# Kernel optimization log

Measured on AMD Instinct MI355X. Metric: run time of the kernel, lower is better.

## Reference

```python
import jax, jax.numpy as jnp
import numpy as np

B, S, D = 4, 2048, 384
H, KVH, HD = 6, 2, 64
GROUPS = H // KVH  # 3
ROPE_THETA = 100000.0


def _rope_tables(seq_len, head_dim, theta):
    inv = 1.0 / (theta ** (np.arange(0, head_dim, 2, dtype=np.float32) / head_dim))
    t = np.arange(seq_len, dtype=np.float32)
    freqs = np.outer(t, inv)  # [S, HD//2]
    return jnp.asarray(np.cos(freqs)), jnp.asarray(np.sin(freqs))


def setup_inputs() -> dict:
    key = jax.random.key(0)
    ks = jax.random.split(key, 5)
    hidden_states = jax.random.normal(ks[0], (B, S, D), dtype=jnp.float32)
    Wq = jax.random.normal(ks[1], (D, H * HD), dtype=jnp.float32) * 0.02
    Wk = jax.random.normal(ks[2], (D, KVH * HD), dtype=jnp.float32) * 0.02
    Wv = jax.random.normal(ks[3], (D, KVH * HD), dtype=jnp.float32) * 0.02
    Wo = jax.random.normal(ks[4], (H * HD, D), dtype=jnp.float32) * 0.02
    freqs_cos, freqs_sin = _rope_tables(S, HD, ROPE_THETA)
    return {"hidden_states": hidden_states, "Wq": Wq, "Wk": Wk, "Wv": Wv,
            "Wo": Wo, "freqs_cos": freqs_cos, "freqs_sin": freqs_sin}


def _apply_rope(x, cos, sin):
    # x: [B, S, h, HD]; treat pairs (even, odd) as complex, multiply by e^{i theta}
    xr = x.reshape(*x.shape[:-1], HD // 2, 2)
    x0, x1 = xr[..., 0], xr[..., 1]
    c = cos[None, :, None, :]  # [1, S, 1, HD//2]
    s = sin[None, :, None, :]
    o0 = x0 * c - x1 * s
    o1 = x0 * s + x1 * c
    return jnp.stack([o0, o1], axis=-1).reshape(x.shape)


def reference(hidden_states, Wq, Wk, Wv, Wo, freqs_cos, freqs_sin):
    Bc, Sc, _ = hidden_states.shape
    q = (hidden_states @ Wq).reshape(Bc, Sc, H, HD)
    k = (hidden_states @ Wk).reshape(Bc, Sc, KVH, HD)
    v = (hidden_states @ Wv).reshape(Bc, Sc, KVH, HD)
    q = _apply_rope(q, freqs_cos, freqs_sin)
    k = _apply_rope(k, freqs_cos, freqs_sin)
    # repeat_interleave over the head dim (GQA group broadcast)
    k = jnp.repeat(k, GROUPS, axis=2)  # [B, S, H, HD]
    v = jnp.repeat(v, GROUPS, axis=2)
    scale = 1.0 / jnp.sqrt(jnp.float32(HD))
    scores = jnp.einsum('bqhd,bkhd->bhqk', q, k) * scale  # [B, H, S, S]
    attn = jax.nn.softmax(scores, axis=-1)
    out = jnp.einsum('bhqk,bkhd->bqhd', attn, v)  # [B, S, H, HD]
    out = out.reshape(Bc, Sc, H * HD)
    return out @ Wo
```

## Files before the change

kernel.cpp:

```cpp
#include <hip/hip_runtime.h>
#include <stdint.h>

#define BATCH   4
#define SEQ     2048
#define DMODEL  384
#define NHEAD   6
#define NKVH    2
#define HD      64
#define MTOK    (BATCH*SEQ)
#define NQKV    640
#define QSCALE  (0.125f * 1.4426950408889634f)

typedef __bf16 bf16x8 __attribute__((ext_vector_type(8)));
typedef float  f32x16 __attribute__((ext_vector_type(16)));

__device__ inline unsigned short f2bf(float f) {
  union { float f; unsigned int u; } v; v.f = f;
  return (unsigned short)((v.u + 0x7fffu + ((v.u >> 16) & 1u)) >> 16);
}
__device__ inline float bf2f(unsigned short b) {
  union { unsigned int u; float f; } v; v.u = ((unsigned int)b) << 16;
  return v.f;
}
__device__ inline unsigned int pack2bf(float a, float b) {
  return (unsigned int)f2bf(a) | ((unsigned int)f2bf(b) << 16);
}
__device__ inline unsigned int cvtpk(float lo, float hi) {
  unsigned int r;
  asm("v_cvt_pk_bf16_f32 %0, %1, %2" : "=v"(r) : "v"(lo), "v"(hi));
  return r;
}
__device__ inline float exp2_fast(float x) {
  float r;
  asm("v_exp_f32 %0, %1" : "=v"(r) : "v"(x));
  return r;
}

#define GLOAD16(gsrc, ldst) __builtin_amdgcn_global_load_lds( \
    (const __attribute__((address_space(1))) void*)(gsrc), \
    (__attribute__((address_space(3))) void*)(ldst), 16, 0, 0)

#define WAITV8() asm volatile("s_waitcnt vmcnt(8)" ::: "memory")
#define WAITV0() asm volatile("s_waitcnt vmcnt(0)" ::: "memory")

__global__ void prep_kernel(const float* __restrict__ X,
                            const float* __restrict__ Wq, const float* __restrict__ Wk,
                            const float* __restrict__ Wv, const float* __restrict__ Wo,
                            unsigned short* __restrict__ Xb,
                            unsigned short* __restrict__ WT,
                            unsigned short* __restrict__ WoT) {
  int idx = blockIdx.x * 256 + threadIdx.x;
  if (idx < (MTOK*DMODEL)/4) {
    float4 v = ((const float4*)X)[idx];
    union { unsigned short s[4]; uint2 u; } o;
    o.s[0] = f2bf(v.x); o.s[1] = f2bf(v.y); o.s[2] = f2bf(v.z); o.s[3] = f2bf(v.w);
    ((uint2*)Xb)[idx] = o.u;
  } else if (idx < (MTOK*DMODEL)/4 + NQKV*DMODEL) {
    int j = idx - (MTOK*DMODEL)/4;
    int n = j / DMODEL, k = j % DMODEL;
    float val = (n < 384) ? Wq[k*384 + n]
              : (n < 512) ? Wk[k*128 + (n-384)]
                          : Wv[k*128 + (n-512)];
    WT[j] = f2bf(val);
  } else if (idx < (MTOK*DMODEL)/4 + NQKV*DMODEL + DMODEL*DMODEL) {
    int j = idx - (MTOK*DMODEL)/4 - NQKV*DMODEL;
    int n = j / DMODEL, k = j % DMODEL;
    WoT[j] = f2bf(Wo[k*384 + n]);
  }
}

template<int NCOLS, bool OUT_BF16>
__global__ __launch_bounds__(256, 2)
void gemm_kernel(const unsigned short* __restrict__ A,
                 const unsigned short* __restrict__ BT,
                 void* __restrict__ Cout) {
  __shared__ unsigned short ldsA[128*64];
  __shared__ unsigned short ldsB[64*64];
  const int tid = threadIdx.x;
  const int wid = tid >> 6, lane = tid & 63;
  const int g = lane >> 5, l31 = lane & 31;
  const int wm = wid >> 1, wn = wid & 1;
  const int mbase = blockIdx.x * 128, nbase = blockIdx.y * 64;

  f32x16 c[2];
  #pragma unroll
  for (int i = 0; i < 2; ++i)
    #pragma unroll
    for (int r = 0; r < 16; ++r) c[i][r] = 0.f;

  for (int kt = 0; kt < DMODEL; kt += 64) {
    #pragma unroll
    for (int i = 0; i < 4; ++i) {
      int L = ((wid*4 + i) << 10) + lane*16;
      int row = L >> 7;
      int slot = (lane & 7) ^ (row & 7);
      GLOAD16(A + (mbase + row)*DMODEL + kt + slot*8, ((char*)ldsA) + L);
    }
    #pragma unroll
    for (int i = 0; i < 2; ++i) {
      int L = ((wid*2 + i) << 10) + lane*16;
      int row = L >> 7;
      int slot = (lane & 7) ^ (row & 7);
      GLOAD16(BT + (nbase + row)*DMODEL + kt + slot*8, ((char*)ldsB) + L);
    }
    __syncthreads();

    bf16x8 bf[4];
    {
      int row = wn*32 + l31;
      #pragma unroll
      for (int s = 0; s < 4; ++s) {
        int slot = ((s<<1) | g) ^ (row & 7);
        bf[s] = *(const bf16x8*)(((const char*)ldsB) + row*128 + slot*16);
      }
    }
    #pragma unroll
    for (int mt = 0; mt < 2; ++mt) {
      int row = wm*64 + mt*32 + l31;
      #pragma unroll
      for (int s = 0; s < 4; ++s) {
        int slot = ((s<<1) | g) ^ (row & 7);
        bf16x8 af = *(const bf16x8*)(((const char*)ldsA) + row*128 + slot*16);
        c[mt] = __builtin_amdgcn_mfma_f32_32x32x16_bf16(af, bf[s], c[mt], 0, 0, 0);
      }
    }
    __syncthreads();
  }

  #pragma unroll
  for (int mt = 0; mt < 2; ++mt)
    #pragma unroll
    for (int rr = 0; rr < 16; ++rr) {
      int m = mbase + wm*64 + mt*32 + (rr&3) + ((rr>>2)<<3) + (g<<2);
      int n = nbase + wn*32 + l31;
      float val = c[mt][rr];
      if (OUT_BF16) ((unsigned short*)Cout)[m*NCOLS + n] = f2bf(val);
      else          ((float*)Cout)[m*NCOLS + n] = val;
    }
}

__global__ void rope_kernel(unsigned short* __restrict__ qkv,
                            const float* __restrict__ fcos,
                            const float* __restrict__ fsin) {
  int t = blockIdx.x;
  int c = threadIdx.x;
  int s = t & (SEQ-1);
  int i = c & 31, col;
  float scale;
  if (c < 192) { int h = c >> 5;          col = h*64 + 2*i;        scale = QSCALE; }
  else         { int kvh = (c - 192) >> 5; col = 384 + kvh*64 + 2*i; scale = 1.0f; }
  unsigned int w = *(unsigned int*)(qkv + t*NQKV + col);
  float x0 = bf2f((unsigned short)(w & 0xffff));
  float x1 = bf2f((unsigned short)(w >> 16));
  float cs = fcos[s*32 + i], sn = fsin[s*32 + i];
  float o0 = (x0*cs - x1*sn) * scale;
  float o1 = (x0*sn + x1*cs) * scale;
  *(unsigned int*)(qkv + t*NQKV + col) = pack2bf(o0, o1);
}

__global__ void vtrans_kernel(const unsigned short* __restrict__ qkv,
                              unsigned short* __restrict__ VT) {
  __shared__ unsigned short tile[64][72];
  int t = threadIdx.x;
  int s0 = blockIdx.x * 64;
  int kvh = blockIdx.y;
  int b = blockIdx.z;
  #pragma unroll
  for (int p = 0; p < 2; ++p) {
    int row = (t >> 3) + p*32;
    int c8 = t & 7;
    uint4 v = *(const uint4*)(qkv + (size_t)(b*SEQ + s0 + row)*NQKV + 512 + kvh*64 + c8*8);
    *(uint4*)(&tile[row][c8*8]) = v;
  }
  __syncthreads();
  #pragma unroll
  for (int p = 0; p < 2; ++p) {
    int d = (t >> 3) + p*32;
    int sj = t & 7;
    union { unsigned short s[8]; uint4 v; } o;
    #pragma unroll
    for (int u = 0; u < 8; ++u) o.s[u] = tile[sj*8 + u][d];
    *(uint4*)(VT + (size_t)((b*2 + kvh)*64 + d)*SEQ + s0 + sj*8) = o.v;
  }
}

__device__ __forceinline__ void stage_tile(const unsigned short* Kbase,
                                           const unsigned short* Vbase,
                                           int kv0, char* kbuf, char* vbuf, int lane) {
  #pragma unroll
  for (int i = 0; i < 4; ++i) {
    int L = (i << 10) + lane*16;
    int row = L >> 7;
    int slot = (lane & 7) ^ (row & 7);
    GLOAD16(Kbase + (kv0 + row)*NQKV + slot*8, kbuf + L);
  }
  #pragma unroll
  for (int i = 0; i < 4; ++i) {
    int L = (i << 10) + lane*16;
    int row = L >> 6;
    int sl4 = (lane & 3) ^ (row & 3) ^ ((row >> 2) & 3);
    GLOAD16(Vbase + row*SEQ + kv0 + sl4*8, vbuf + L);
  }
}

__global__ __launch_bounds__(128, 2)
void attn_kernel(const unsigned short* __restrict__ qkv,
                 const unsigned short* __restrict__ VT,
                 unsigned short* __restrict__ attnO) {
  __shared__ __align__(16) char smem[32768];
  const int tid = threadIdx.x;
  const int wid = tid >> 6, lane = tid & 63;
  const int g = lane >> 5, l31 = lane & 31;

  int bid = blockIdx.x;
  int e = (bid & 7)*192 + (bid >> 3);
  int qt = e & 63;
  int hb = e >> 6;
  int h = hb % 6, b = hb / 6;
  const int kvh = h / 3;
  const int token = b*SEQ + qt*32 + l31;
  const int kvbase = wid * (SEQ/2);

  char* kb0 = smem + wid*16384;
  char* vb0 = kb0 + 4096;

  bf16x8 qf[4];
  #pragma unroll
  for (int s = 0; s < 4; ++s)
    qf[s] = *(const bf16x8*)(qkv + (size_t)token*NQKV + h*64 + s*16 + g*8);

  f32x16 acc0, acc1;
  #pragma unroll
  for (int r = 0; r < 16; ++r) { acc0[r] = 0.f; acc1[r] = 0.f; }
  float m = -1e30f, l = 0.f;

  const unsigned short* Kbase = qkv + (size_t)(b*SEQ)*NQKV + 384 + kvh*64;
  const unsigned short* Vbase = VT + (size_t)((b*2 + kvh)*64)*SEQ;

  stage_tile(Kbase, Vbase, kvbase, kb0, vb0, lane);

  for (int t = 0; t < 32; ++t) {
    int cur = t & 1;
    if (t < 31)
      stage_tile(Kbase, Vbase, kvbase + (t+1)*32,
                 kb0 + ((t+1)&1)*8192, vb0 + ((t+1)&1)*8192, lane);
    if (t < 31) { WAITV8(); } else { WAITV0(); }

    const char* kb = kb0 + cur*8192;
    const char* vb = vb0 + cur*8192;

    f32x16 c1;
    #pragma unroll
    for (int r = 0; r < 16; ++r) c1[r] = 0.f;
    {
      int row = l31;
      #pragma unroll
      for (int s = 0; s < 4; ++s) {
        int slot = ((s<<1) | g) ^ (row & 7);
        bf16x8 kf = *(const bf16x8*)(kb + row*128 + slot*16);
        c1 = __builtin_amdgcn_mfma_f32_32x32x16_bf16(kf, qf[s], c1, 0, 0, 0);
      }
    }

    float pmax = c1[0];
    #pragma unroll
    for (int r = 1; r < 16; ++r) pmax = fmaxf(pmax, c1[r]);
    pmax = fmaxf(pmax, __shfl_xor(pmax, 32));
    if (!__all(pmax <= m + 10.f)) {
      float mnew = fmaxf(m, pmax);
      float alpha = exp2_fast(m - mnew);
      #pragma unroll
      for (int r = 0; r < 16; ++r) { acc0[r] *= alpha; acc1[r] *= alpha; }
      l *= alpha;
      m = mnew;
    }
    float p[16]; float psum = 0.f;
    #pragma unroll
    for (int r = 0; r < 16; ++r) {
      p[r] = exp2_fast(c1[r] - m);
      psum += p[r];
    }
    l += psum;

    #pragma unroll
    for (int sl = 0; sl < 2; ++sl) {
      int rb = sl*8;
      unsigned int w0  = cvtpk(p[rb+0], p[rb+1]);
      unsigned int w1  = cvtpk(p[rb+2], p[rb+3]);
      unsigned int wh0 = cvtpk(p[rb+4], p[rb+5]);
      unsigned int wh1 = cvtpk(p[rb+6], p[rb+7]);
      unsigned int s0 = g ? w0 : wh0;
      unsigned int s1 = g ? w1 : wh1;
      unsigned int r0 = __shfl_xor(s0, 32);
      unsigned int r1 = __shfl_xor(s1, 32);
      union { bf16x8 v; unsigned int u[4]; } pf;
      pf.u[0] = g ? r0  : w0;
      pf.u[1] = g ? r1  : w1;
      pf.u[2] = g ? wh0 : r0;
      pf.u[3] = g ? wh1 : r1;
      #pragma unroll
      for (int dt = 0; dt < 2; ++dt) {
        int row = dt*32 + l31;
        int t16 = (sl*2 + g) ^ (row & 3) ^ ((row >> 2) & 3);
        bf16x8 vf = *(const bf16x8*)(vb + row*64 + t16*16);
        if (dt == 0) acc0 = __builtin_amdgcn_mfma_f32_32x32x16_bf16(vf, pf.v, acc0, 0, 0, 0);
        else         acc1 = __builtin_amdgcn_mfma_f32_32x32x16_bf16(vf, pf.v, acc1, 0, 0, 0);
      }
    }
  }

  l += __shfl_xor(l, 32);
  __syncthreads();
  float* cmb  = (float*)smem;
  float* accx = (float*)(smem + 512);
  if (g == 0) { cmb[wid*64 + l31] = m; cmb[wid*64 + 32 + l31] = l; }
  __syncthreads();
  int ow = wid ^ 1;
  float m_o = cmb[ow*64 + l31], l_o = cmb[ow*64 + 32 + l31];
  float ms = fmaxf(m, m_o);
  float a = exp2_fast(m - ms);
  if (wid == 1) {
    #pragma unroll
    for (int dt = 0; dt < 2; ++dt)
      #pragma unroll
      for (int r = 0; r < 16; ++r) {
        int d = dt*32 + (r&3) + ((r>>2)<<3) + (g<<2);
        accx[d*32 + l31] = (dt ? acc1[r] : acc0[r]) * a;
      }
  }
  __syncthreads();
  if (wid == 0) {
    float a_o = exp2_fast(m_o - ms);
    float lstar = l*a + l_o*a_o;
    float invl = 1.0f / lstar;
    #pragma unroll
    for (int dt = 0; dt < 2; ++dt)
      #pragma unroll
      for (int q8 = 0; q8 < 4; ++q8) {
        union { unsigned short s[4]; uint2 u; } ov;
        #pragma unroll
        for (int j = 0; j < 4; ++j) {
          int r = q8*4 + j;
          int d = dt*32 + (r&3) + ((r>>2)<<3) + (g<<2);
          float tot = (dt ? acc1[r] : acc0[r])*a + accx[d*32 + l31];
          ov.s[j] = f2bf(tot * invl);
        }
        int d0 = dt*32 + q8*8 + g*4;
        *(uint2*)(attnO + (size_t)token*DMODEL + h*64 + d0) = ov.u;
      }
  }
}

extern "C" void kernel_launch(void* const* d_in, const int* in_sizes, int n_in,
                              void* d_out, int out_size, void* d_ws, size_t ws_size,
                              hipStream_t stream) {
  const float* X    = (const float*)d_in[0];
  const float* Wq   = (const float*)d_in[1];
  const float* Wk   = (const float*)d_in[2];
  const float* Wv   = (const float*)d_in[3];
  const float* Wo   = (const float*)d_in[4];
  const float* fcos = (const float*)d_in[5];
  const float* fsin = (const float*)d_in[6];
  char* ws = (char*)d_ws;

  unsigned short* Xb    = (unsigned short*)(ws);
  unsigned short* QKV   = (unsigned short*)(ws + 6291456);
  unsigned short* VTb   = (unsigned short*)(ws + 16777216);
  unsigned short* attnO = (unsigned short*)(ws + 18874368);
  unsigned short* WT    = (unsigned short*)(ws + 25165824);
  unsigned short* WoT   = (unsigned short*)(ws + 25657344);

  prep_kernel<<<4608, 256, 0, stream>>>(X, Wq, Wk, Wv, Wo, Xb, WT, WoT);
  gemm_kernel<NQKV, true><<<dim3(64, 10), 256, 0, stream>>>(Xb, WT, QKV);
  rope_kernel<<<MTOK, 256, 0, stream>>>(QKV, fcos, fsin);
  vtrans_kernel<<<dim3(32, 2, 4), 256, 0, stream>>>(QKV, VTb);
  attn_kernel<<<1536, 128, 0, stream>>>(QKV, VTb, attnO);
  gemm_kernel<DMODEL, false><<<dim3(64, 6), 256, 0, stream>>>(attnO, WoT, (void*)d_out);
}
```

Measured before the change: 177.4 us.

## Fuse RoPE into QKV GEMM, split attention into per-wave blocks with combine kernel

Applies RoPE and the Q scale in the QKV GEMM epilogue, with a lane shuffle to fetch the pair partner, which removes the separate rope kernel and its round trip through memory. V is rearranged into MFMA-fragment order so the attention kernel loads V fragments straight into registers, prefetched one tile ahead, and stages only K through LDS. The two-wave block with LDS merging becomes a one-wave block over a 2-way KV split grid. Partial outputs (stored as bf16) and the running max and sum go to global memory and a new combine kernel merges them, at the cost of an extra launch, extra traffic and an extra bf16 rounding.

```diff
diff --git a/kernel.cpp b/kernel.cpp
--- a/kernel.cpp
+++ b/kernel.cpp
@@ -22,9 +22,6 @@
   union { unsigned int u; float f; } v; v.u = ((unsigned int)b) << 16;
   return v.f;
 }
-__device__ inline unsigned int pack2bf(float a, float b) {
-  return (unsigned int)f2bf(a) | ((unsigned int)f2bf(b) << 16);
-}
 __device__ inline unsigned int cvtpk(float lo, float hi) {
   unsigned int r;
   asm("v_cvt_pk_bf16_f32 %0, %1, %2" : "=v"(r) : "v"(lo), "v"(hi));
@@ -39,9 +36,6 @@
 #define GLOAD16(gsrc, ldst) __builtin_amdgcn_global_load_lds( \
     (const __attribute__((address_space(1))) void*)(gsrc), \
     (__attribute__((address_space(3))) void*)(ldst), 16, 0, 0)
-
-#define WAITV8() asm volatile("s_waitcnt vmcnt(8)" ::: "memory")
-#define WAITV0() asm volatile("s_waitcnt vmcnt(0)" ::: "memory")
 
 __global__ void prep_kernel(const float* __restrict__ X,
                             const float* __restrict__ Wq, const float* __restrict__ Wk,
@@ -69,11 +63,13 @@
   }
 }
 
-template<int NCOLS, bool OUT_BF16>
+template<int NCOLS, bool OUT_BF16, bool ROPE>
 __global__ __launch_bounds__(256, 2)
 void gemm_kernel(const unsigned short* __restrict__ A,
                  const unsigned short* __restrict__ BT,
-                 void* __restrict__ Cout) {
+                 void* __restrict__ Cout,
+                 const float* __restrict__ fcos,
+                 const float* __restrict__ fsin) {
   __shared__ unsigned short ldsA[128*64];
   __shared__ unsigned short ldsB[64*64];
   const int tid = threadIdx.x;
@@ -127,39 +123,32 @@
     __syncthreads();
   }
 
+  const int n = nbase + wn*32 + l31;
+  const bool isqk = ROPE && (nbase < 512);
+  const float rscale = (nbase < 384) ? QSCALE : 1.0f;
+  const int ri = (n & 63) >> 1;
+  const bool odd = (n & 1) != 0;
+
   #pragma unroll
   for (int mt = 0; mt < 2; ++mt)
     #pragma unroll
     for (int rr = 0; rr < 16; ++rr) {
       int m = mbase + wm*64 + mt*32 + (rr&3) + ((rr>>2)<<3) + (g<<2);
-      int n = nbase + wn*32 + l31;
       float val = c[mt][rr];
+      if (isqk) {
+        float xp = __shfl_xor(val, 1);
+        int s = m & (SEQ-1);
+        float cs = fcos[s*32 + ri], sn = fsin[s*32 + ri];
+        val = odd ? (xp*sn + val*cs) : (val*cs - xp*sn);
+        val *= rscale;
+      }
       if (OUT_BF16) ((unsigned short*)Cout)[m*NCOLS + n] = f2bf(val);
       else          ((float*)Cout)[m*NCOLS + n] = val;
     }
 }
 
-__global__ void rope_kernel(unsigned short* __restrict__ qkv,
-                            const float* __restrict__ fcos,
-                            const float* __restrict__ fsin) {
-  int t = blockIdx.x;
-  int c = threadIdx.x;
-  int s = t & (SEQ-1);
-  int i = c & 31, col;
-  float scale;
-  if (c < 192) { int h = c >> 5;          col = h*64 + 2*i;        scale = QSCALE; }
-  else         { int kvh = (c - 192) >> 5; col = 384 + kvh*64 + 2*i; scale = 1.0f; }
-  unsigned int w = *(unsigned int*)(qkv + t*NQKV + col);
-  float x0 = bf2f((unsigned short)(w & 0xffff));
-  float x1 = bf2f((unsigned short)(w >> 16));
-  float cs = fcos[s*32 + i], sn = fsin[s*32 + i];
-  float o0 = (x0*cs - x1*sn) * scale;
-  float o1 = (x0*sn + x1*cs) * scale;
-  *(unsigned int*)(qkv + t*NQKV + col) = pack2bf(o0, o1);
-}
-
-__global__ void vtrans_kernel(const unsigned short* __restrict__ qkv,
-                              unsigned short* __restrict__ VT) {
+__global__ void vfrag_kernel(const unsigned short* __restrict__ qkv,
+                             unsigned short* __restrict__ Vf) {
   __shared__ unsigned short tile[64][72];
   int t = threadIdx.x;
   int s0 = blockIdx.x * 64;
@@ -173,56 +162,123 @@
     *(uint4*)(&tile[row][c8*8]) = v;
   }
   __syncthreads();
+  unsigned short* base = Vf + (size_t)(b*2 + kvh)*131072;
   #pragma unroll
   for (int p = 0; p < 2; ++p) {
-    int d = (t >> 3) + p*32;
-    int sj = t & 7;
+    int c = t + p*256;
+    int tloc = c >> 8;
+    int r = c & 255;
+    int dt = r >> 7, sl = (r >> 6) & 1, lane = r & 63;
+    int gg = lane >> 5, ll = lane & 31;
     union { unsigned short s[8]; uint4 v; } o;
     #pragma unroll
-    for (int u = 0; u < 8; ++u) o.s[u] = tile[sj*8 + u][d];
-    *(uint4*)(VT + (size_t)((b*2 + kvh)*64 + d)*SEQ + s0 + sj*8) = o.v;
-  }
-}
-
-__device__ __forceinline__ void stage_tile(const unsigned short* Kbase,
-                                           const unsigned short* Vbase,
-                                           int kv0, char* kbuf, char* vbuf, int lane) {
+    for (int j = 0; j < 8; ++j)
+      o.s[j] = tile[tloc*32 + sl*16 + gg*8 + j][dt*32 + ll];
+    *(uint4*)(base + (size_t)(s0/32 + tloc)*2048 + (dt*2 + sl)*512 + lane*8) = o.v;
+  }
+}
+
+__device__ __forceinline__ void stage_k(const unsigned short* Kbase, int kv0,
+                                        char* kbuf, int lane) {
   #pragma unroll
   for (int i = 0; i < 4; ++i) {
     int L = (i << 10) + lane*16;
     int row = L >> 7;
     int slot = (lane & 7) ^ (row & 7);
-    GLOAD16(Kbase + (kv0 + row)*NQKV + slot*8, kbuf + L);
-  }
-  #pragma unroll
-  for (int i = 0; i < 4; ++i) {
-    int L = (i << 10) + lane*16;
-    int row = L >> 6;
-    int sl4 = (lane & 3) ^ (row & 3) ^ ((row >> 2) & 3);
-    GLOAD16(Vbase + row*SEQ + kv0 + sl4*8, vbuf + L);
-  }
-}
-
-__global__ __launch_bounds__(128, 2)
+    GLOAD16(Kbase + (size_t)(kv0 + row)*NQKV + slot*8, kbuf + L);
+  }
+}
+
+#define ATTN_BODY(T, VC0, VC1, VC2, VC3, VN0, VN1, VN2, VN3, PREF) do {            \
+  if (PREF) {                                                                      \
+    stage_k(Kbase, kvbase + ((T)+1)*32, kbuf + (((T)+1)&1)*4096, lane);            \
+    const unsigned short* vp = Vfb + (size_t)(part*32 + (T)+1)*2048;               \
+    VN0 = *(const bf16x8*)(vp + lane*8);                                           \
+    VN1 = *(const bf16x8*)(vp + 512 + lane*8);                                     \
+    VN2 = *(const bf16x8*)(vp + 1024 + lane*8);                                    \
+    VN3 = *(const bf16x8*)(vp + 1536 + lane*8);                                    \
+    asm volatile("s_waitcnt vmcnt(8)" ::: "memory");                               \
+  } else {                                                                         \
+    asm volatile("s_waitcnt vmcnt(0)" ::: "memory");                               \
+  }                                                                                \
+  const char* kb = kbuf + ((T)&1)*4096;                                            \
+  f32x16 c1;                                                                       \
+  _Pragma("unroll")                                                                \
+  for (int r = 0; r < 16; ++r) c1[r] = 0.f;                                        \
+  _Pragma("unroll")                                                                \
+  for (int s = 0; s < 4; ++s) {                                                    \
+    int slot = ((s<<1) | g) ^ (l31 & 7);                                           \
+    bf16x8 kf = *(const bf16x8*)(kb + l31*128 + slot*16);                          \
+    c1 = __builtin_amdgcn_mfma_f32_32x32x16_bf16(kf, qf[s], c1, 0, 0, 0);          \
+  }                                                                                \
+  float x0 = fmaxf(c1[0],c1[1]), x1 = fmaxf(c1[2],c1[3]);                          \
+  float x2 = fmaxf(c1[4],c1[5]), x3 = fmaxf(c1[6],c1[7]);                          \
+  float x4 = fmaxf(c1[8],c1[9]), x5 = fmaxf(c1[10],c1[11]);                        \
+  float x6 = fmaxf(c1[12],c1[13]), x7 = fmaxf(c1[14],c1[15]);                      \
+  float y0 = fmaxf(x0,x1), y1 = fmaxf(x2,x3), y2 = fmaxf(x4,x5), y3 = fmaxf(x6,x7);\
+  float pmax = fmaxf(fmaxf(y0,y1), fmaxf(y2,y3));                                  \
+  pmax = fmaxf(pmax, __shfl_xor(pmax, 32));                                        \
+  if (!__all(pmax <= mrun + 10.f)) {                                               \
+    float mnew = fmaxf(mrun, pmax);                                                \
+    float alpha = exp2_fast(mrun - mnew);                                          \
+    _Pragma("unroll")                                                              \
+    for (int r = 0; r < 16; ++r) { acc0[r] *= alpha; acc1[r] *= alpha; }           \
+    lrun *= alpha;                                                                 \
+    mrun = mnew;                                                                   \
+  }                                                                                \
+  float p[16];                                                                     \
+  _Pragma("unroll")                                                                \
+  for (int r = 0; r < 16; ++r) p[r] = exp2_fast(c1[r] - mrun);                     \
+  {                                                                                \
+    float s0_ = (p[0]+p[1])+(p[2]+p[3]), s1_ = (p[4]+p[5])+(p[6]+p[7]);            \
+    float s2_ = (p[8]+p[9])+(p[10]+p[11]), s3_ = (p[12]+p[13])+(p[14]+p[15]);      \
+    lrun += (s0_+s1_)+(s2_+s3_);                                                   \
+  }                                                                                \
+  _Pragma("unroll")                                                                \
+  for (int sl = 0; sl < 2; ++sl) {                                                 \
+    int rb = sl*8;                                                                 \
+    unsigned int w0  = cvtpk(p[rb+0], p[rb+1]);                                    \
+    unsigned int w1  = cvtpk(p[rb+2], p[rb+3]);                                    \
+    unsigned int wh0 = cvtpk(p[rb+4], p[rb+5]);                                    \
+    unsigned int wh1 = cvtpk(p[rb+6], p[rb+7]);                                    \
+    unsigned int t0 = g ? w0 : wh0;                                                \
+    unsigned int t1 = g ? w1 : wh1;                                                \
+    unsigned int r0 = __shfl_xor(t0, 32);                                          \
+    unsigned int r1 = __shfl_xor(t1, 32);                                          \
+    union { bf16x8 v; unsigned int u[4]; } pf;                                     \
+    pf.u[0] = g ? r0  : w0;                                                        \
+    pf.u[1] = g ? r1  : w1;                                                        \
+    pf.u[2] = g ? wh0 : r0;                                                        \
+    pf.u[3] = g ? wh1 : r1;                                                        \
+    if (sl == 0) {                                                                 \
+      acc0 = __builtin_amdgcn_mfma_f32_32x32x16_bf16(VC0, pf.v, acc0, 0, 0, 0);    \
+      acc1 = __builtin_amdgcn_mfma_f32_32x32x16_bf16(VC2, pf.v, acc1, 0, 0, 0);    \
+    } else {                                                                       \
+      acc0 = __builtin_amdgcn_mfma_f32_32x32x16_bf16(VC1, pf.v, acc0, 0, 0, 0);    \
+      acc1 = __builtin_amdgcn_mfma_f32_32x32x16_bf16(VC3, pf.v, acc1, 0, 0, 0);    \
+    }                                                                              \
+  }                                                                                \
+} while (0)
+
+__global__ __launch_bounds__(64, 3)
 void attn_kernel(const unsigned short* __restrict__ qkv,
-                 const unsigned short* __restrict__ VT,
-                 unsigned short* __restrict__ attnO) {
-  __shared__ __align__(16) char smem[32768];
-  const int tid = threadIdx.x;
-  const int wid = tid >> 6, lane = tid & 63;
+                 const unsigned short* __restrict__ Vf,
+                 unsigned short* __restrict__ PO0,
+                 unsigned short* __restrict__ PO1,
+                 float2* __restrict__ ML) {
+  __shared__ __align__(16) char kbuf[8192];
+  const int lane = threadIdx.x;
   const int g = lane >> 5, l31 = lane & 31;
 
   int bid = blockIdx.x;
+  const int part = blockIdx.y;
   int e = (bid & 7)*192 + (bid >> 3);
   int qt = e & 63;
   int hb = e >> 6;
   int h = hb % 6, b = hb / 6;
   const int kvh = h / 3;
   const int token = b*SEQ + qt*32 + l31;
-  const int kvbase = wid * (SEQ/2);
-
-  char* kb0 = smem + wid*16384;
-  char* vb0 = kb0 + 4096;
+  const int kvbase = part * (SEQ/2);
 
   bf16x8 qf[4];
   #pragma unroll
@@ -232,123 +288,69 @@
   f32x16 acc0, acc1;
   #pragma unroll
   for (int r = 0; r < 16; ++r) { acc0[r] = 0.f; acc1[r] = 0.f; }
-  float m = -1e30f, l = 0.f;
+  float mrun = -1e30f, lrun = 0.f;
 
   const unsigned short* Kbase = qkv + (size_t)(b*SEQ)*NQKV + 384 + kvh*64;
-  const unsigned short* Vbase = VT + (size_t)((b*2 + kvh)*64)*SEQ;
-
-  stage_tile(Kbase, Vbase, kvbase, kb0, vb0, lane);
-
-  for (int t = 0; t < 32; ++t) {
-    int cur = t & 1;
-    if (t < 31)
-      stage_tile(Kbase, Vbase, kvbase + (t+1)*32,
-                 kb0 + ((t+1)&1)*8192, vb0 + ((t+1)&1)*8192, lane);
-    if (t < 31) { WAITV8(); } else { WAITV0(); }
-
-    const char* kb = kb0 + cur*8192;
-    const char* vb = vb0 + cur*8192;
-
-    f32x16 c1;
-    #pragma unroll
-    for (int r = 0; r < 16; ++r) c1[r] = 0.f;
-    {
-      int row = l31;
+  const unsigned short* Vfb = Vf + (size_t)(b*2 + kvh)*131072;
+
+  bf16x8 vA0, vA1, vA2, vA3, vB0, vB1, vB2, vB3;
+
+  stage_k(Kbase, kvbase, kbuf, lane);
+  {
+    const unsigned short* vp = Vfb + (size_t)(part*32)*2048;
+    vA0 = *(const bf16x8*)(vp + lane*8);
+    vA1 = *(const bf16x8*)(vp + 512 + lane*8);
+    vA2 = *(const bf16x8*)(vp + 1024 + lane*8);
+    vA3 = *(const bf16x8*)(vp + 1536 + lane*8);
+  }
+
+  for (int tt = 0; tt < 30; tt += 2) {
+    ATTN_BODY(tt,   vA0, vA1, vA2, vA3, vB0, vB1, vB2, vB3, true);
+    ATTN_BODY(tt+1, vB0, vB1, vB2, vB3, vA0, vA1, vA2, vA3, true);
+  }
+  ATTN_BODY(30, vA0, vA1, vA2, vA3, vB0, vB1, vB2, vB3, true);
+  ATTN_BODY(31, vB0, vB1, vB2, vB3, vA0, vA1, vA2, vA3, false);
+
+  lrun += __shfl_xor(lrun, 32);
+  unsigned short* PO = part ? PO1 : PO0;
+  #pragma unroll
+  for (int dt = 0; dt < 2; ++dt)
+    #pragma unroll
+    for (int q8 = 0; q8 < 4; ++q8) {
+      union { unsigned short s[4]; uint2 u; } ov;
       #pragma unroll
-      for (int s = 0; s < 4; ++s) {
-        int slot = ((s<<1) | g) ^ (row & 7);
-        bf16x8 kf = *(const bf16x8*)(kb + row*128 + slot*16);
-        c1 = __builtin_amdgcn_mfma_f32_32x32x16_bf16(kf, qf[s], c1, 0, 0, 0);
+      for (int j = 0; j < 4; ++j) {
+        int r = q8*4 + j;
+        ov.s[j] = f2bf(dt ? acc1[r] : acc0[r]);
       }
-    }
-
-    float pmax = c1[0];
-    #pragma unroll
-    for (int r = 1; r < 16; ++r) pmax = fmaxf(pmax, c1[r]);
-    pmax = fmaxf(pmax, __shfl_xor(pmax, 32));
-    if (!__all(pmax <= m + 10.f)) {
-      float mnew = fmaxf(m, pmax);
-      float alpha = exp2_fast(m - mnew);
-      #pragma unroll
-      for (int r = 0; r < 16; ++r) { acc0[r] *= alpha; acc1[r] *= alpha; }
-      l *= alpha;
-      m = mnew;
-    }
-    float p[16]; float psum = 0.f;
-    #pragma unroll
-    for (int r = 0; r < 16; ++r) {
-      p[r] = exp2_fast(c1[r] - m);
-      psum += p[r];
-    }
-    l += psum;
-
-    #pragma unroll
-    for (int sl = 0; sl < 2; ++sl) {
-      int rb = sl*8;
-      unsigned int w0  = cvtpk(p[rb+0], p[rb+1]);
-      unsigned int w1  = cvtpk(p[rb+2], p[rb+3]);
-      unsigned int wh0 = cvtpk(p[rb+4], p[rb+5]);
-      unsigned int wh1 = cvtpk(p[rb+6], p[rb+7]);
-      unsigned int s0 = g ? w0 : wh0;
-      unsigned int s1 = g ? w1 : wh1;
-      unsigned int r0 = __shfl_xor(s0, 32);
-      unsigned int r1 = __shfl_xor(s1, 32);
-      union { bf16x8 v; unsigned int u[4]; } pf;
-      pf.u[0] = g ? r0  : w0;
-      pf.u[1] = g ? r1  : w1;
-      pf.u[2] = g ? wh0 : r0;
-      pf.u[3] = g ? wh1 : r1;
-      #pragma unroll
-      for (int dt = 0; dt < 2; ++dt) {
-        int row = dt*32 + l31;
-        int t16 = (sl*2 + g) ^ (row & 3) ^ ((row >> 2) & 3);
-        bf16x8 vf = *(const bf16x8*)(vb + row*64 + t16*16);
-        if (dt == 0) acc0 = __builtin_amdgcn_mfma_f32_32x32x16_bf16(vf, pf.v, acc0, 0, 0, 0);
-        else         acc1 = __builtin_amdgcn_mfma_f32_32x32x16_bf16(vf, pf.v, acc1, 0, 0, 0);
-      }
-    }
-  }
-
-  l += __shfl_xor(l, 32);
-  __syncthreads();
-  float* cmb  = (float*)smem;
-  float* accx = (float*)(smem + 512);
-  if (g == 0) { cmb[wid*64 + l31] = m; cmb[wid*64 + 32 + l31] = l; }
-  __syncthreads();
-  int ow = wid ^ 1;
-  float m_o = cmb[ow*64 + l31], l_o = cmb[ow*64 + 32 + l31];
-  float ms = fmaxf(m, m_o);
-  float a = exp2_fast(m - ms);
-  if (wid == 1) {
-    #pragma unroll
-    for (int dt = 0; dt < 2; ++dt)
-      #pragma unroll
-      for (int r = 0; r < 16; ++r) {
-        int d = dt*32 + (r&3) + ((r>>2)<<3) + (g<<2);
-        accx[d*32 + l31] = (dt ? acc1[r] : acc0[r]) * a;
-      }
-  }
-  __syncthreads();
-  if (wid == 0) {
-    float a_o = exp2_fast(m_o - ms);
-    float lstar = l*a + l_o*a_o;
-    float invl = 1.0f / lstar;
-    #pragma unroll
-    for (int dt = 0; dt < 2; ++dt)
-      #pragma unroll
-      for (int q8 = 0; q8 < 4; ++q8) {
-        union { unsigned short s[4]; uint2 u; } ov;
-        #pragma unroll
-        for (int j = 0; j < 4; ++j) {
-          int r = q8*4 + j;
-          int d = dt*32 + (r&3) + ((r>>2)<<3) + (g<<2);
-          float tot = (dt ? acc1[r] : acc0[r])*a + accx[d*32 + l31];
-          ov.s[j] = f2bf(tot * invl);
-        }
-        int d0 = dt*32 + q8*8 + g*4;
-        *(uint2*)(attnO + (size_t)token*DMODEL + h*64 + d0) = ov.u;
-      }
-  }
+      int d = dt*32 + q8*8 + g*4;
+      *(uint2*)(PO + (size_t)token*DMODEL + h*64 + d) = ov.u;
+    }
+  if (g == 0)
+    ML[(size_t)part*49152 + token*6 + h] = make_float2(mrun, lrun);
+}
+
+__global__ void combine_kernel(const unsigned short* __restrict__ PO0,
+                               const unsigned short* __restrict__ PO1,
+                               const float2* __restrict__ ML,
+                               unsigned short* __restrict__ attnO) {
+  int idx = blockIdx.x*256 + threadIdx.x;
+  int token = idx / 48;
+  int c8 = idx - token*48;
+  int h = c8 >> 3;
+  float2 ml0 = ML[token*6 + h];
+  float2 ml1 = ML[49152 + token*6 + h];
+  float M = fmaxf(ml0.x, ml1.x);
+  float a0 = exp2_fast(ml0.x - M), a1 = exp2_fast(ml1.x - M);
+  float inv = 1.0f / (ml0.y*a0 + ml1.y*a1);
+  float s0 = a0*inv, s1 = a1*inv;
+  union { unsigned short s[8]; uint4 v; } p0, p1, o;
+  p0.v = *(const uint4*)(PO0 + (size_t)idx*8);
+  p1.v = *(const uint4*)(PO1 + (size_t)idx*8);
+  #pragma unroll
+  for (int j = 0; j < 8; ++j)
+    o.s[j] = f2bf(bf2f(p0.s[j])*s0 + bf2f(p1.s[j])*s1);
+  *(uint4*)(attnO + (size_t)idx*8) = o.v;
 }
 
 extern "C" void kernel_launch(void* const* d_in, const int* in_sizes, int n_in,
@@ -364,16 +366,19 @@
   char* ws = (char*)d_ws;
 
   unsigned short* Xb    = (unsigned short*)(ws);
+  unsigned short* PO0   = (unsigned short*)(ws);
   unsigned short* QKV   = (unsigned short*)(ws + 6291456);
-  unsigned short* VTb   = (unsigned short*)(ws + 16777216);
+  unsigned short* Vf    = (unsigned short*)(ws + 16777216);
   unsigned short* attnO = (unsigned short*)(ws + 18874368);
   unsigned short* WT    = (unsigned short*)(ws + 25165824);
   unsigned short* WoT   = (unsigned short*)(ws + 25657344);
+  unsigned short* PO1   = (unsigned short*)(ws + 25952256);
+  float2*         ML    = (float2*)       (ws + 32243712);
 
   prep_kernel<<<4608, 256, 0, stream>>>(X, Wq, Wk, Wv, Wo, Xb, WT, WoT);
-  gemm_kernel<NQKV, true><<<dim3(64, 10), 256, 0, stream>>>(Xb, WT, QKV);
-  rope_kernel<<<MTOK, 256, 0, stream>>>(QKV, fcos, fsin);
-  vtrans_kernel<<<dim3(32, 2, 4), 256, 0, stream>>>(QKV, VTb);
-  attn_kernel<<<1536, 128, 0, stream>>>(QKV, VTb, attnO);
-  gemm_kernel<DMODEL, false><<<dim3(64, 6), 256, 0, stream>>>(attnO, WoT, (void*)d_out);
-}
+  gemm_kernel<NQKV, true, true><<<dim3(64, 10), 256, 0, stream>>>(Xb, WT, QKV, fcos, fsin);
+  vfrag_kernel<<<dim3(32, 2, 4), 256, 0, stream>>>(QKV, Vf);
+  attn_kernel<<<dim3(1536, 2), 64, 0, stream>>>(QKV, Vf, PO0, PO1, ML);
+  combine_kernel<<<1536, 256, 0, stream>>>(PO0, PO1, ML, attnO);
+  gemm_kernel<DMODEL, false, false><<<dim3(64, 6), 256, 0, stream>>>(attnO, WoT, (void*)d_out, nullptr, nullptr);
+}
```

Result: faster. 155.0 us (-12.6%).
